# Kernel optimization log

Hardware: AMD Instinct MI355X
Metric: run time of the kernel (lower is better)

## Reference

```python
import jax, jax.numpy as jnp
import numpy as np

B, S, D, H = 4, 2048, 2048, 16
HD = D // H            # 128 head dim
HID = 5632             # SwiGLU hidden: multiple_of*ceil((2/3*4*D)/multiple_of)
EPS = 1e-6


def setup_inputs() -> dict:
    key = jax.random.key(0)
    ks = jax.random.split(key, 12)
    s = 0.02
    x = jax.random.normal(ks[0], (B, S, D), dtype=jnp.float32)
    # RoPE freqs (theta=10000), complex freqs_cis represented as cos/sin
    inv_freq = 1.0 / (10000.0 ** (np.arange(0, HD, 2, dtype=np.float32) / HD))
    t = np.arange(S, dtype=np.float32)
    ang = np.outer(t, inv_freq)                      # [S, HD/2]
    freqs_cos = jnp.asarray(np.cos(ang), dtype=jnp.float32)
    freqs_sin = jnp.asarray(np.sin(ang), dtype=jnp.float32)
    # additive causal mask [1,1,S,S]
    mask = jnp.where(jnp.triu(jnp.ones((S, S), dtype=bool), k=1), -jnp.inf, 0.0)
    mask = mask.astype(jnp.float32)[None, None]
    return {
        "x": x,
        "freqs_cos": freqs_cos,
        "freqs_sin": freqs_sin,
        "mask": mask,
        "wq": jax.random.normal(ks[1], (D, D), jnp.float32) * s,
        "wk": jax.random.normal(ks[2], (D, D), jnp.float32) * s,
        "wv": jax.random.normal(ks[3], (D, D), jnp.float32) * s,
        "wo": jax.random.normal(ks[4], (D, D), jnp.float32) * s,
        "w1": jax.random.normal(ks[5], (HID, D), jnp.float32) * s,
        "w2": jax.random.normal(ks[6], (D, HID), jnp.float32) * s,
        "w3": jax.random.normal(ks[7], (HID, D), jnp.float32) * s,
        "attn_norm_w": jnp.ones((D,), jnp.float32),
        "ffn_norm_w": jnp.ones((D,), jnp.float32),
        "start_pos": 0,
    }


def rmsnorm(x, w, eps=EPS):
    xf = x.astype(jnp.float32)
    y = xf * jax.lax.rsqrt(jnp.mean(xf * xf, axis=-1, keepdims=True) + eps)
    return y.astype(x.dtype) * w


def apply_rope(q, k, cos, sin):
    # q,k: [B,S,H,HD]; cos,sin: [S,HD/2]
    def rot(x):
        xf = x.astype(jnp.float32).reshape(*x.shape[:-1], HD // 2, 2)
        xr, xi = xf[..., 0], xf[..., 1]
        c = cos[None, :, None, :]
        s = sin[None, :, None, :]
        out = jnp.stack([xr * c - xi * s, xr * s + xi * c], axis=-1)
        return out.reshape(*x.shape).astype(x.dtype)
    return rot(q), rot(k)


def reference(x, freqs_cos, freqs_sin, mask, wq, wk, wv, wo, w1, w2, w3,
              attn_norm_w, ffn_norm_w, start_pos):
    # ---- attention ----
    xa = rmsnorm(x, attn_norm_w)
    q = (xa @ wq.T).reshape(B, S, H, HD)
    k = (xa @ wk.T).reshape(B, S, H, HD)
    v = (xa @ wv.T).reshape(B, S, H, HD)
    q, k = apply_rope(q, k, freqs_cos, freqs_sin)
    # [B,H,S,S] scores (naive, materialized as in original)
    scores = jnp.einsum('bqhd,bkhd->bhqk', q, k) / jnp.sqrt(jnp.float32(HD))
    scores = scores + mask
    attn = jax.nn.softmax(scores, axis=-1)
    o = jnp.einsum('bhqk,bkhd->bqhd', attn, v).reshape(B, S, D)
    h = x + o @ wo.T
    # ---- SwiGLU FFN ----
    hf = rmsnorm(h, ffn_norm_w)
    ff = (jax.nn.silu(hf @ w1.T) * (hf @ w3.T)) @ w2.T
    return h + ff
```

## Files before the change

### kernel.cpp

```cpp
#include <hip/hip_runtime.h>
#include <hip/hip_bf16.h>
#include <stdint.h>

typedef short  bf16x8_t __attribute__((ext_vector_type(8)));
typedef short  bf16x4_t __attribute__((ext_vector_type(4)));
typedef float  f32x4_t  __attribute__((ext_vector_type(4)));
typedef unsigned short u16;
typedef unsigned int   u32;

#define DEV __device__ __forceinline__

DEV u16 f2bf(float f){
  u32 u = __float_as_uint(f);
  u += 0x7fffu + ((u >> 16) & 1u);
  return (u16)(u >> 16);
}
DEV float bf2f(u16 h){ return __uint_as_float(((u32)h) << 16); }

DEV void gl16(const void* g, void* l){
  __builtin_amdgcn_global_load_lds(
      (const __attribute__((address_space(1))) void*)g,
      (__attribute__((address_space(3))) void*)l, 16, 0, 0);
}

#define SBAR() do{ __builtin_amdgcn_sched_barrier(0); __builtin_amdgcn_s_barrier(); \
                   __builtin_amdgcn_sched_barrier(0); }while(0)

__global__ __launch_bounds__(256) void cvt_k(const float* __restrict__ in,
                                             u16* __restrict__ out, int n8){
  int i = blockIdx.x * 256 + threadIdx.x;
  if (i >= n8) return;
  const float4* p = (const float4*)in;
  float4 a = p[(size_t)i*2], b = p[(size_t)i*2+1];
  bf16x8_t o;
  o[0]=(short)f2bf(a.x); o[1]=(short)f2bf(a.y); o[2]=(short)f2bf(a.z); o[3]=(short)f2bf(a.w);
  o[4]=(short)f2bf(b.x); o[5]=(short)f2bf(b.y); o[6]=(short)f2bf(b.z); o[7]=(short)f2bf(b.w);
  *(bf16x8_t*)(out + (size_t)i*8) = o;
}

__global__ __launch_bounds__(256) void rmsnorm_k(const float* __restrict__ x,
                                                 const float* __restrict__ w,
                                                 u16* __restrict__ y){
  int row = blockIdx.x, t = threadIdx.x;
  const float4* xr = (const float4*)(x + (size_t)row*2048);
  float4 a = xr[t*2], b = xr[t*2+1];
  float ss = a.x*a.x+a.y*a.y+a.z*a.z+a.w*a.w + b.x*b.x+b.y*b.y+b.z*b.z+b.w*b.w;
  #pragma unroll
  for (int m = 32; m; m >>= 1) ss += __shfl_xor(ss, m, 64);
  __shared__ float red[4];
  if ((t & 63) == 0) red[t >> 6] = ss;
  __syncthreads();
  float tot = red[0]+red[1]+red[2]+red[3];
  float rs = rsqrtf(tot * (1.0f/2048.0f) + 1e-6f);
  const float4* wr = (const float4*)w;
  float4 wa = wr[t*2], wb = wr[t*2+1];
  bf16x8_t o;
  o[0]=(short)f2bf(a.x*rs*wa.x); o[1]=(short)f2bf(a.y*rs*wa.y);
  o[2]=(short)f2bf(a.z*rs*wa.z); o[3]=(short)f2bf(a.w*rs*wa.w);
  o[4]=(short)f2bf(b.x*rs*wb.x); o[5]=(short)f2bf(b.y*rs*wb.y);
  o[6]=(short)f2bf(b.z*rs*wb.z); o[7]=(short)f2bf(b.w*rs*wb.w);
  *(bf16x8_t*)(y + (size_t)row*2048 + t*8) = o;
}

__global__ __launch_bounds__(256) void rmsnorm2_k(const float* __restrict__ x,
                                                  const u16* __restrict__ t1,
                                                  const float* __restrict__ w,
                                                  u16* __restrict__ y){
  int row = blockIdx.x, t = threadIdx.x;
  const float4* xr = (const float4*)(x + (size_t)row*2048);
  float4 a = xr[t*2], b = xr[t*2+1];
  bf16x8_t tv = *(const bf16x8_t*)(t1 + (size_t)row*2048 + t*8);
  float h[8];
  h[0]=a.x+bf2f((u16)tv[0]); h[1]=a.y+bf2f((u16)tv[1]);
  h[2]=a.z+bf2f((u16)tv[2]); h[3]=a.w+bf2f((u16)tv[3]);
  h[4]=b.x+bf2f((u16)tv[4]); h[5]=b.y+bf2f((u16)tv[5]);
  h[6]=b.z+bf2f((u16)tv[6]); h[7]=b.w+bf2f((u16)tv[7]);
  float ss = 0.f;
  #pragma unroll
  for (int j=0;j<8;j++) ss += h[j]*h[j];
  #pragma unroll
  for (int m = 32; m; m >>= 1) ss += __shfl_xor(ss, m, 64);
  __shared__ float red[4];
  if ((t & 63) == 0) red[t >> 6] = ss;
  __syncthreads();
  float tot = red[0]+red[1]+red[2]+red[3];
  float rs = rsqrtf(tot * (1.0f/2048.0f) + 1e-6f);
  const float4* wr = (const float4*)w;
  float4 wa = wr[t*2], wb = wr[t*2+1];
  bf16x8_t o;
  o[0]=(short)f2bf(h[0]*rs*wa.x); o[1]=(short)f2bf(h[1]*rs*wa.y);
  o[2]=(short)f2bf(h[2]*rs*wa.z); o[3]=(short)f2bf(h[3]*rs*wa.w);
  o[4]=(short)f2bf(h[4]*rs*wb.x); o[5]=(short)f2bf(h[5]*rs*wb.y);
  o[6]=(short)f2bf(h[6]*rs*wb.z); o[7]=(short)f2bf(h[7]*rs*wb.w);
  *(bf16x8_t*)(y + (size_t)row*2048 + t*8) = o;
}

__global__ __launch_bounds__(256) void rope_k(u16* __restrict__ q, u16* __restrict__ k,
                                              const float* __restrict__ fc,
                                              const float* __restrict__ fs){
  int i = blockIdx.x * 256 + threadIdx.x;
  int ii = i & 63; int h = (i >> 6) & 15; int bs = i >> 10;
  int s = bs & 2047;
  size_t off = (size_t)bs*2048 + h*128 + 2*ii;
  float c = fc[s*64+ii], sn = fs[s*64+ii];
  u32 qq = *(u32*)(q + off);
  float xr = bf2f((u16)(qq & 0xffff)), xi = bf2f((u16)(qq >> 16));
  *(u32*)(q + off) = (u32)f2bf(xr*c - xi*sn) | ((u32)f2bf(xr*sn + xi*c) << 16);
  u32 kk = *(u32*)(k + off);
  xr = bf2f((u16)(kk & 0xffff)); xi = bf2f((u16)(kk >> 16));
  *(u32*)(k + off) = (u32)f2bf(xr*c - xi*sn) | ((u32)f2bf(xr*sn + xi*c) << 16);
}

__global__ __launch_bounds__(256) void transpose_k(const u16* __restrict__ in,
                                                   u16* __restrict__ out){
  __shared__ u16 tile[64*68];
  int tid = threadIdx.x;
  int tm = blockIdx.x >> 5, tn = blockIdx.x & 31;
  const u16* src = in + (size_t)(tm*64)*2048 + tn*64;
  #pragma unroll
  for (int i=0;i<2;i++){
    int idx = i*256 + tid;
    int r = idx >> 3, c8 = (idx & 7)*8;
    *(bf16x8_t*)&tile[r*68 + c8] = *(const bf16x8_t*)(src + (size_t)r*2048 + c8);
  }
  __syncthreads();
  u16* dst = out + (size_t)(tn*64)*8192 + tm*64;
  #pragma unroll
  for (int i=0;i<2;i++){
    int idx = i*256 + tid;
    int oc = idx >> 3, r8 = (idx & 7)*8;
    bf16x8_t v;
    #pragma unroll
    for (int j=0;j<8;j++) v[j] = tile[(r8+j)*68 + oc];
    *(bf16x8_t*)(dst + (size_t)oc*8192 + r8) = v;
  }
}


DEV void stg(const u16* __restrict__ G, int K, u16* dst, int tid, int Toff){
  #pragma unroll
  for (int j=0;j<2;j++){
    int c = j*512 + tid;
    int row = c >> 2;
    int l = (c&3) ^ ((row>>1)&3);
    gl16(G + (size_t)row*K + Toff + l*8, dst + (size_t)c*8);
  }
}

template<int MH, bool LOADB>
DEV void phase_mm(const u16* baseA, const u16* baseB, int l15, int pc,
                  int wm, int wn, bf16x8_t (&bf)[4], f32x4_t (&acc)[8][4]){
  bf16x8_t af[4];
  #pragma unroll
  for (int mi=0; mi<4; mi++){
    int R = wm*128 + MH*64 + mi*16 + l15;
    af[mi] = *(const bf16x8_t*)&baseA[R*32 + pc];
  }
  if (LOADB){
    #pragma unroll
    for (int ni=0; ni<4; ni++){
      int Rb = wn*64 + ni*16 + l15;
      bf[ni] = *(const bf16x8_t*)&baseB[Rb*32 + pc];
    }
  }
  asm volatile("s_waitcnt lgkmcnt(0)" ::: "memory");
  __builtin_amdgcn_sched_barrier(0);
  __builtin_amdgcn_s_setprio(1);
  #pragma unroll
  for (int mi=0; mi<4; mi++)
    #pragma unroll
    for (int ni=0; ni<4; ni++)
      acc[MH*4+mi][ni] =
        __builtin_amdgcn_mfma_f32_16x16x32_bf16(af[mi], bf[ni], acc[MH*4+mi][ni], 0,0,0);
  __builtin_amdgcn_s_setprio(0);
}

template<int EPI>
__global__ __launch_bounds__(512, 2) void gemm_bt(const u16* __restrict__ A,
                                                  const u16* __restrict__ B,
                                                  void* __restrict__ C,
                                                  const void* __restrict__ aux,
                                                  const void* __restrict__ aux2,
                                                  int M, int N, int K){
  __shared__ __align__(16) u16 sA[2*2*8192];
  __shared__ __align__(16) u16 sB[2*2*8192];
  int tid = threadIdx.x, lane = tid & 63, wave = tid >> 6;
  int l15 = lane & 15, l4 = lane >> 4;
  int pc = (l4 ^ ((l15 >> 1) & 3)) * 8;
  int nbn = N / 256;
  int nwg = gridDim.x, bid = blockIdx.x;
  int qq = nwg >> 3, rr = nwg & 7;
  int xc = bid & 7, yy = bid >> 3;
  int wg = (xc < rr ? xc*(qq+1) : rr*(qq+1) + (xc-rr)*qq) + yy;
  int tm = wg / nbn, tn = wg % nbn;
  size_t m0 = (size_t)tm*256, n0 = (size_t)tn*256;
  const u16* Ag = A + m0*K;
  const u16* Bg = B + n0*K;
  int wm = wave >> 2, wn = wave & 3;

  f32x4_t acc[8][4];
  #pragma unroll
  for (int i=0;i<8;i++)
    #pragma unroll
    for (int j=0;j<4;j++)
      acc[i][j] = (f32x4_t){0.f,0.f,0.f,0.f};
  bf16x8_t bf[4];

  int nk = K / 64;
  stg(Ag, K, &sA[0],     tid, 0);
  stg(Bg, K, &sB[0],     tid, 0);
  stg(Ag, K, &sA[8192],  tid, 32);
  stg(Bg, K, &sB[8192],  tid, 32);
  stg(Ag, K, &sA[16384], tid, 64);
  stg(Bg, K, &sB[16384], tid, 64);

  for (int T=0; T<nk; ++T){
    int buf = T & 1, bufn = buf ^ 1;
    const u16* A0 = &sA[buf*16384];
    const u16* B0 = &sB[buf*16384];
    if (T+1 < nk) asm volatile("s_waitcnt vmcnt(8)" ::: "memory");
    else          asm volatile("s_waitcnt vmcnt(4)" ::: "memory");
    SBAR();
    if (T+1 < nk) stg(Ag, K, &sA[bufn*16384 + 8192], tid, (T+1)*64 + 32);
    phase_mm<0,true >(A0,        B0,        l15, pc, wm, wn, bf, acc);
    SBAR();
    if (T+1 < nk) stg(Bg, K, &sB[bufn*16384 + 8192], tid, (T+1)*64 + 32);
    phase_mm<1,false>(A0,        B0,        l15, pc, wm, wn, bf, acc);
    if (T+1 < nk) asm volatile("s_waitcnt vmcnt(8)" ::: "memory");
    else          asm volatile("s_waitcnt vmcnt(0)" ::: "memory");
    SBAR();
    if (T+2 < nk) stg(Ag, K, &sA[buf*16384], tid, (T+2)*64);
    phase_mm<0,true >(A0+8192,   B0+8192,   l15, pc, wm, wn, bf, acc);
    SBAR();
    if (T+2 < nk) stg(Bg, K, &sB[buf*16384], tid, (T+2)*64);
    phase_mm<1,false>(A0+8192,   B0+8192,   l15, pc, wm, wn, bf, acc);
  }

  #pragma unroll
  for (int am=0; am<8; am++)
    #pragma unroll
    for (int ni=0; ni<4; ni++)
      #pragma unroll
      for (int r=0; r<4; r++){
        float v = acc[am][ni][r];
        size_t rowg = m0 + am*16 + wm*128 + l4*4 + r;
        size_t colg = n0 + wn*64 + ni*16 + l15;
        size_t idx = rowg * (size_t)N + colg;
        if constexpr (EPI == 0){
          ((u16*)C)[idx] = f2bf(v);
        } else if constexpr (EPI == 1){
          float s = v / (1.0f + __expf(-v));
          ((u16*)C)[idx] = f2bf(s);
        } else if constexpr (EPI == 2){
          float a = bf2f(((const u16*)aux)[idx]);
          ((u16*)C)[idx] = f2bf(v * a);
        } else {
          float a = ((const float*)aux)[idx];
          float b2 = bf2f(((const u16*)aux2)[idx]);
          ((float*)C)[idx] = v + a + b2;
        }
      }
}

__global__ __launch_bounds__(256) void attn_k(const u16* __restrict__ Q,
                                              const u16* __restrict__ K,
                                              const u16* __restrict__ VT,
                                              u16* __restrict__ O){
  __shared__ __align__(16) u16 sK[32*128];
  __shared__ __align__(16) u16 sVT[128*32];
  int tid = threadIdx.x, lane = tid & 63, wave = tid >> 6;
  int bid = blockIdx.x;
  int qt = 31 - (bid >> 6);
  int bh = bid & 63; int b = bh >> 4, h = bh & 15;
  int l15 = lane & 15, l4 = lane >> 4;
  size_t base = ((size_t)b*2048)*2048 + (size_t)h*128;
  const u16* VTg0 = VT + ((size_t)h*128)*8192 + (size_t)b*2048;
  int qr0 = qt*64 + wave*16;
  int qrow = qr0 + l15;
  bf16x8_t qf[4];
  #pragma unroll
  for (int s=0;s<4;s++)
    qf[s] = *(const bf16x8_t*)(Q + base + (size_t)qrow*2048 + s*32 + l4*8);

  f32x4_t oaccT[8];
  #pragma unroll
  for (int f=0;f<8;f++) oaccT[f] = (f32x4_t){0.f,0.f,0.f,0.f};
  float mrun = -1e30f, lrun = 0.f;

  const float scale = 0.08838834764831845f;
  int nkt = (qt + 1) * 2;
  for (int kt=0; kt<nkt; ++kt){
    __syncthreads();
    const u16* Kg = K + base + (size_t)kt*32*2048;
    #pragma unroll
    for (int i=0;i<2;i++){
      int c = i*256 + tid; int row = c>>4;
      gl16(Kg + (size_t)row*2048 + (size_t)(((c&15) ^ (row&7))*8), &sK[c*8]);
    }
    #pragma unroll
    for (int i=0;i<2;i++){
      int c = i*256 + tid; int d = c>>2;
      gl16(VTg0 + (size_t)d*8192 + kt*32 + (size_t)((((c&3) ^ ((d>>1)&3)))*8),
           &sVT[c*8]);
    }
    __syncthreads();

    if (kt*32 <= qr0 + 15){
      f32x4_t sacc[2];
      sacc[0] = (f32x4_t){0.f,0.f,0.f,0.f};
      sacc[1] = (f32x4_t){0.f,0.f,0.f,0.f};
      __builtin_amdgcn_s_setprio(1);
      #pragma unroll
      for (int n=0;n<2;n++)
        #pragma unroll
        for (int s=0;s<4;s++){
          bf16x8_t kf = *(const bf16x8_t*)
              &sK[(n*16 + l15)*128 + (((s*4 + l4) ^ (l15 & 7))*8)];
          sacc[n] = __builtin_amdgcn_mfma_f32_16x16x32_bf16(kf, qf[s], sacc[n], 0,0,0);
        }
      __builtin_amdgcn_s_setprio(0);
      float pv[8];
      float mloc = -1e30f;
      #pragma unroll
      for (int n=0;n<2;n++)
        #pragma unroll
        for (int r=0;r<4;r++){
          int kg = kt*32 + n*16 + l4*4 + r;
          float v = sacc[n][r] * scale;
          if (kg > qrow) v = -1e30f;
          pv[n*4+r] = v;
          mloc = fmaxf(mloc, v);
        }
      mloc = fmaxf(mloc, __shfl_xor(mloc, 16, 64));
      mloc = fmaxf(mloc, __shfl_xor(mloc, 32, 64));
      float mnew = fmaxf(mrun, mloc);
      float fr = __expf(mrun - mnew);
      mrun = mnew;
      float sloc = 0.f;
      bf16x8_t pa;
      #pragma unroll
      for (int j=0;j<8;j++){
        float p = __expf(pv[j] - mnew);
        sloc += p;
        pa[j] = (short)f2bf(p);
      }
      sloc += __shfl_xor(sloc, 16, 64);
      sloc += __shfl_xor(sloc, 32, 64);
      lrun = lrun * fr + sloc;
      #pragma unroll
      for (int f=0;f<8;f++){
        oaccT[f][0] *= fr; oaccT[f][1] *= fr; oaccT[f][2] *= fr; oaccT[f][3] *= fr;
      }
      __builtin_amdgcn_s_setprio(1);
      #pragma unroll
      for (int f=0;f<8;f++){
        int d = f*16 + l15;
        bf16x4_t lo = *(const bf16x4_t*)&sVT[d*32 + (((0*4 + l4) ^ (d & 6))*4)];
        bf16x4_t hi = *(const bf16x4_t*)&sVT[d*32 + (((1*4 + l4) ^ (d & 6))*4)];
        bf16x8_t va;
        va[0]=lo[0]; va[1]=lo[1]; va[2]=lo[2]; va[3]=lo[3];
        va[4]=hi[0]; va[5]=hi[1]; va[6]=hi[2]; va[7]=hi[3];
        oaccT[f] = __builtin_amdgcn_mfma_f32_16x16x32_bf16(va, pa, oaccT[f], 0,0,0);
      }
      __builtin_amdgcn_s_setprio(0);
    }
  }
  float inv = 1.0f / lrun;
  size_t orow = (size_t)b*2048 + qrow;
  #pragma unroll
  for (int f=0;f<8;f++){
    bf16x4_t ov;
    ov[0]=(short)f2bf(oaccT[f][0]*inv); ov[1]=(short)f2bf(oaccT[f][1]*inv);
    ov[2]=(short)f2bf(oaccT[f][2]*inv); ov[3]=(short)f2bf(oaccT[f][3]*inv);
    *(bf16x4_t*)(O + orow*2048 + h*128 + f*16 + l4*4) = ov;
  }
}

extern "C" void kernel_launch(void* const* d_in, const int* in_sizes, int n_in,
                              void* d_out, int out_size, void* d_ws, size_t ws_size,
                              hipStream_t stream){
  (void)in_sizes; (void)n_in; (void)out_size; (void)ws_size;
  const float* x   = (const float*)d_in[0];
  const float* fc  = (const float*)d_in[1];
  const float* fs  = (const float*)d_in[2];
  const float* wq  = (const float*)d_in[4];
  const float* wk  = (const float*)d_in[5];
  const float* wv  = (const float*)d_in[6];
  const float* wo  = (const float*)d_in[7];
  const float* w1  = (const float*)d_in[8];
  const float* w2  = (const float*)d_in[9];
  const float* w3  = (const float*)d_in[10];
  const float* anw = (const float*)d_in[11];
  const float* fnw = (const float*)d_in[12];
  float* out = (float*)d_out;
  char* ws = (char*)d_ws;

  const int M = 8192, D = 2048, HID = 5632;
  const size_t WB   = 23068672ull;
  const size_t ACT2 = 33554432ull;

  u16* wbuf = (u16*)(ws);
  u16* xa   = (u16*)(ws + WB);
  u16* qb   = (u16*)(ws + WB + ACT2);
  u16* kb   = (u16*)(ws + WB + 2*ACT2);
  u16* vb   = (u16*)(ws + WB + 3*ACT2);
  u16* g1   = (u16*)(ws + WB + 4*ACT2);
  u16* vt = g1;
  u16* t1 = qb;
  u16* hf = kb;

  rmsnorm_k<<<M, 256, 0, stream>>>(x, anw, xa);

  cvt_k<<<D*D/8/256, 256, 0, stream>>>(wq, wbuf, D*D/8);
  gemm_bt<0><<<(M/256)*(D/256), 512, 0, stream>>>(xa, wbuf, qb, nullptr, nullptr, M, D, D);
  cvt_k<<<D*D/8/256, 256, 0, stream>>>(wk, wbuf, D*D/8);
  gemm_bt<0><<<(M/256)*(D/256), 512, 0, stream>>>(xa, wbuf, kb, nullptr, nullptr, M, D, D);
  cvt_k<<<D*D/8/256, 256, 0, stream>>>(wv, wbuf, D*D/8);
  gemm_bt<0><<<(M/256)*(D/256), 512, 0, stream>>>(xa, wbuf, vb, nullptr, nullptr, M, D, D);

  rope_k<<<32768, 256, 0, stream>>>(qb, kb, fc, fs);
  transpose_k<<<4096, 256, 0, stream>>>(vb, vt);

  attn_k<<<2048, 256, 0, stream>>>(qb, kb, vt, xa);

  cvt_k<<<D*D/8/256, 256, 0, stream>>>(wo, wbuf, D*D/8);
  gemm_bt<0><<<(M/256)*(D/256), 512, 0, stream>>>(xa, wbuf, t1, nullptr, nullptr, M, D, D);

  rmsnorm2_k<<<M, 256, 0, stream>>>(x, t1, fnw, hf);

  cvt_k<<<HID*D/8/256, 256, 0, stream>>>(w1, wbuf, HID*D/8);
  gemm_bt<1><<<(M/256)*(HID/256), 512, 0, stream>>>(hf, wbuf, g1, nullptr, nullptr, M, HID, D);
  cvt_k<<<HID*D/8/256, 256, 0, stream>>>(w3, wbuf, HID*D/8);
  gemm_bt<2><<<(M/256)*(HID/256), 512, 0, stream>>>(hf, wbuf, g1, g1, nullptr, M, HID, D);
  cvt_k<<<HID*D/8/256, 256, 0, stream>>>(w2, wbuf, HID*D/8);
  gemm_bt<4><<<(M/256)*(D/256), 512, 0, stream>>>(g1, wbuf, out, x, t1, M, D, HID);
}
```

Baseline: 1.323 ms.

## Software-pipeline LDS fragment reads against MFMAs and halve GEMM barriers

Restructures the bf16 GEMM main loop so that the LDS reads for the next sub-tile's A/B fragments are issued while the MFMAs for the current sub-tile run. The first fragments of the next K-step are prefetched at the end of each iteration. A and B global-to-LDS stages are now issued together, so there are two block barriers per K-step instead of four, with adjusted vmcnt waits. The aim is to hide LDS latency and cut synchronisation stalls, at the cost of more live fragment registers, which could pressure occupancy at 512 threads x2.

After: 1.318 ms. No clear change (-0.4%).

```diff
diff --git a/kernel.cpp b/kernel.cpp
--- a/kernel.cpp
+++ b/kernel.cpp
@@ -23,8 +23,8 @@
       (__attribute__((address_space(3))) void*)l, 16, 0, 0);
 }
 
-#define SBAR() do{ __builtin_amdgcn_sched_barrier(0); __builtin_amdgcn_s_barrier(); \
-                   __builtin_amdgcn_sched_barrier(0); }while(0)
+#define SB0() __builtin_amdgcn_sched_barrier(0)
+#define BARF() do{ SB0(); __builtin_amdgcn_s_barrier(); SB0(); }while(0)
 
 __global__ __launch_bounds__(256) void cvt_k(const float* __restrict__ in,
                                              u16* __restrict__ out, int n8){
@@ -147,31 +147,30 @@
   }
 }
 
-template<int MH, bool LOADB>
-DEV void phase_mm(const u16* baseA, const u16* baseB, int l15, int pc,
-                  int wm, int wn, bf16x8_t (&bf)[4], f32x4_t (&acc)[8][4]){
-  bf16x8_t af[4];
-  #pragma unroll
-  for (int mi=0; mi<4; mi++){
-    int R = wm*128 + MH*64 + mi*16 + l15;
-    af[mi] = *(const bf16x8_t*)&baseA[R*32 + pc];
-  }
-  if (LOADB){
-    #pragma unroll
-    for (int ni=0; ni<4; ni++){
-      int Rb = wn*64 + ni*16 + l15;
-      bf[ni] = *(const bf16x8_t*)&baseB[Rb*32 + pc];
-    }
-  }
-  asm volatile("s_waitcnt lgkmcnt(0)" ::: "memory");
-  __builtin_amdgcn_sched_barrier(0);
+DEV void rdA(const u16* base, int wm, int mh, int l15, int pc, bf16x8_t (&r)[4]){
+  #pragma unroll
+  for (int mi=0;mi<4;mi++){
+    int R = wm*128 + mh*64 + mi*16 + l15;
+    r[mi] = *(const bf16x8_t*)&base[R*32 + pc];
+  }
+}
+DEV void rdB(const u16* base, int wn, int l15, int pc, bf16x8_t (&r)[4]){
+  #pragma unroll
+  for (int ni=0;ni<4;ni++){
+    int R = wn*64 + ni*16 + l15;
+    r[ni] = *(const bf16x8_t*)&base[R*32 + pc];
+  }
+}
+
+template<int MH>
+DEV void MM16(bf16x8_t (&a)[4], bf16x8_t (&b)[4], f32x4_t (&acc)[8][4]){
   __builtin_amdgcn_s_setprio(1);
   #pragma unroll
-  for (int mi=0; mi<4; mi++)
-    #pragma unroll
-    for (int ni=0; ni<4; ni++)
+  for (int mi=0;mi<4;mi++)
+    #pragma unroll
+    for (int ni=0;ni<4;ni++)
       acc[MH*4+mi][ni] =
-        __builtin_amdgcn_mfma_f32_16x16x32_bf16(af[mi], bf[ni], acc[MH*4+mi][ni], 0,0,0);
+        __builtin_amdgcn_mfma_f32_16x16x32_bf16(a[mi], b[ni], acc[MH*4+mi][ni], 0,0,0);
   __builtin_amdgcn_s_setprio(0);
 }
 
@@ -204,36 +203,51 @@
     #pragma unroll
     for (int j=0;j<4;j++)
       acc[i][j] = (f32x4_t){0.f,0.f,0.f,0.f};
-  bf16x8_t bf[4];
 
   int nk = K / 64;
-  stg(Ag, K, &sA[0],     tid, 0);
-  stg(Bg, K, &sB[0],     tid, 0);
-  stg(Ag, K, &sA[8192],  tid, 32);
-  stg(Bg, K, &sB[8192],  tid, 32);
-  stg(Ag, K, &sA[16384], tid, 64);
-  stg(Bg, K, &sB[16384], tid, 64);
+  stg(Ag, K, &sA[0],     tid, 0);  stg(Bg, K, &sB[0],     tid, 0);
+  stg(Ag, K, &sA[8192],  tid, 32); stg(Bg, K, &sB[8192],  tid, 32);
+  stg(Ag, K, &sA[16384], tid, 64); stg(Bg, K, &sB[16384], tid, 64);
+  asm volatile("s_waitcnt vmcnt(8)" ::: "memory");
+  BARF();
+  bf16x8_t aA[4], bA[4], aB[4], aC[4], aD[4], bB[4];
+  rdA(&sA[0], wm, 0, l15, pc, aA);
+  rdB(&sB[0], wn, l15, pc, bA);
+  SB0();
 
   for (int T=0; T<nk; ++T){
-    int buf = T & 1, bufn = buf ^ 1;
-    const u16* A0 = &sA[buf*16384];
-    const u16* B0 = &sB[buf*16384];
-    if (T+1 < nk) asm volatile("s_waitcnt vmcnt(8)" ::: "memory");
-    else          asm volatile("s_waitcnt vmcnt(4)" ::: "memory");
-    SBAR();
-    if (T+1 < nk) stg(Ag, K, &sA[bufn*16384 + 8192], tid, (T+1)*64 + 32);
-    phase_mm<0,true >(A0,        B0,        l15, pc, wm, wn, bf, acc);
-    SBAR();
-    if (T+1 < nk) stg(Bg, K, &sB[bufn*16384 + 8192], tid, (T+1)*64 + 32);
-    phase_mm<1,false>(A0,        B0,        l15, pc, wm, wn, bf, acc);
-    if (T+1 < nk) asm volatile("s_waitcnt vmcnt(8)" ::: "memory");
+    int cb = T & 1, nb = cb ^ 1;
+    const u16* Ac0 = &sA[cb*16384]; const u16* Ac1 = Ac0 + 8192;
+    const u16* Bc0 = &sB[cb*16384]; const u16* Bc1 = Bc0 + 8192;
+    if (T < nk-1) asm volatile("s_waitcnt vmcnt(4)" ::: "memory");
     else          asm volatile("s_waitcnt vmcnt(0)" ::: "memory");
-    SBAR();
-    if (T+2 < nk) stg(Ag, K, &sA[buf*16384], tid, (T+2)*64);
-    phase_mm<0,true >(A0+8192,   B0+8192,   l15, pc, wm, wn, bf, acc);
-    SBAR();
-    if (T+2 < nk) stg(Bg, K, &sB[buf*16384], tid, (T+2)*64);
-    phase_mm<1,false>(A0+8192,   B0+8192,   l15, pc, wm, wn, bf, acc);
+    BARF();
+    if (T+1 < nk){
+      stg(Ag, K, &sA[nb*16384 + 8192], tid, (T+1)*64 + 32);
+      stg(Bg, K, &sB[nb*16384 + 8192], tid, (T+1)*64 + 32);
+    }
+    SB0();
+    rdA(Ac0, wm, 1, l15, pc, aB); SB0();
+    MM16<0>(aA, bA, acc);
+    rdA(Ac1, wm, 0, l15, pc, aC);
+    rdB(Bc1, wn, l15, pc, bB); SB0();
+    MM16<1>(aB, bA, acc);
+    rdA(Ac1, wm, 1, l15, pc, aD); SB0();
+    MM16<0>(aC, bB, acc);
+    if (T < nk-1) asm volatile("s_waitcnt vmcnt(4)" ::: "memory");
+    else          asm volatile("s_waitcnt vmcnt(0)" ::: "memory");
+    BARF();
+    if (T+2 < nk){
+      stg(Ag, K, &sA[cb*16384], tid, (T+2)*64);
+      stg(Bg, K, &sB[cb*16384], tid, (T+2)*64);
+    }
+    SB0();
+    MM16<1>(aD, bB, acc);
+    if (T+1 < nk){
+      rdA(&sA[nb*16384], wm, 0, l15, pc, aA);
+      rdB(&sB[nb*16384], wn, l15, pc, bA);
+    }
+    SB0();
   }
 
   #pragma unroll
@@ -243,7 +257,7 @@
       #pragma unroll
       for (int r=0; r<4; r++){
         float v = acc[am][ni][r];
-        size_t rowg = m0 + am*16 + wm*128 + l4*4 + r;
+        size_t rowg = m0 + (am&3)*16 + (am>>2)*64 + wm*128 + l4*4 + r;
         size_t colg = n0 + wn*64 + ni*16 + l15;
         size_t idx = rowg * (size_t)N + colg;
         if constexpr (EPI == 0){
```
